# Performance work log

Measured on AMD Instinct MI355X. Metric: run time of the kernel, lower is better.

The kernel has to match this reference:

```python
import jax, jax.numpy as jnp
import numpy as np

NHEADS = 2
STRENGTH = 0.1
ZED = 8  # zone_embed_dim
STATE_DIM = 137
HID = 256
NBLOCKS = 4
BATCH = 131072


def _mha_seq1(q, k, v, in_w, in_b, out_w, out_b):
    """nn.MultiheadAttention (batch_first) with q,k,v of shape [B,1,E]."""
    B, _, E = q.shape
    hd = E // NHEADS
    Wq, Wk, Wv = in_w[:E], in_w[E:2 * E], in_w[2 * E:]
    bq, bk, bv = in_b[:E], in_b[E:2 * E], in_b[2 * E:]

    def heads(x, W, b):
        return (x @ W.T + b).reshape(B, -1, NHEADS, hd).transpose(0, 2, 1, 3)  # [B,H,1,hd]

    qh, kh, vh = heads(q, Wq, bq), heads(k, Wk, bk), heads(v, Wv, bv)
    scale = 1.0 / jnp.sqrt(jnp.asarray(hd, q.dtype))
    s = jnp.einsum('bhqd,bhkd->bhqk', qh, kh) * scale
    a = jax.nn.softmax(s, axis=-1)  # trivially ones for kv_len=1, kept for fidelity
    o = jnp.einsum('bhqk,bhkd->bhqd', a, vh).transpose(0, 2, 1, 3).reshape(B, -1, E)
    return o @ out_w.T + out_b


def setup_inputs() -> dict:
    key = jax.random.key(0)
    ks = jax.random.split(key, 20)
    S, H, N = STATE_DIM, HID, NBLOCKS
    ahd = S - ZED - 1  # 128

    def w(k, shape, fan_in):
        return jax.random.normal(k, shape, jnp.float32) * (1.0 / np.sqrt(fan_in))

    inp = {
        't': jax.random.uniform(ks[0], (1,), jnp.float32) * 24.0,
        'state': jax.random.normal(ks[1], (BATCH, S), jnp.float32),
        'W0': w(ks[2], (H, S + 2), S + 2), 'b0': jnp.zeros((H,), jnp.float32),
        'blkW1': w(ks[3], (N, H, H), H), 'blkb1': jnp.zeros((N, H), jnp.float32),
        'blkW2': w(ks[4], (N, H, H), H), 'blkb2': jnp.zeros((N, H), jnp.float32),
        'Wout': w(ks[5], (S, H), H), 'bout': jnp.zeros((S,), jnp.float32),
        'lm_in_w': w(ks[6], (3 * ZED, ZED), ZED), 'lm_in_b': jnp.zeros((3 * ZED,), jnp.float32),
        'lm_out_w': w(ks[7], (ZED, ZED), ZED), 'lm_out_b': jnp.zeros((ZED,), jnp.float32),
        'ta_in_w': w(ks[8], (3 * ahd, ahd), ahd), 'ta_in_b': jnp.zeros((3 * ahd,), jnp.float32),
        'ta_out_w': w(ks[9], (ahd, ahd), ahd), 'ta_out_b': jnp.zeros((ahd,), jnp.float32),
    }
    return inp


def reference(t, state, W0, b0, blkW1, blkb1, blkW2, blkb2, Wout, bout,
              lm_in_w, lm_in_b, lm_out_w, lm_out_b,
              ta_in_w, ta_in_b, ta_out_w, ta_out_b):
    B, S = state.shape
    ahd = S - ZED - 1
    two_pi_over_24 = 2.0 * jnp.pi / 24.0
    tv = jnp.concatenate([jnp.sin(t * two_pi_over_24), jnp.cos(t * two_pi_over_24)])  # [2]
    t_vec = jnp.broadcast_to(tv, (B, 2))

    # core dynamics MLP: Linear -> ReLU -> residual blocks -> Linear
    x = jnp.concatenate([state, t_vec], axis=-1)
    h = jax.nn.relu(x @ W0.T + b0)
    for i in range(blkW1.shape[0]):
        inner = jnp.tanh(h @ blkW1[i].T + blkb1[i]) @ blkW2[i].T + blkb2[i]
        h = jnp.tanh(h + inner)
    core = h @ Wout.T + bout

    # attention delta
    hs = state[:, :ahd]
    loc = state[:, ahd:ahd + ZED]
    mov = state[:, -1:]

    q_lm = jnp.broadcast_to(mov, (B, ZED))[:, None, :]
    loc_e = loc[:, None, :]
    enh_loc = _mha_seq1(q_lm, loc_e, loc_e, lm_in_w, lm_in_b, lm_out_w, lm_out_b)[:, 0]
    delta_loc = enh_loc - loc

    t_pad = jnp.concatenate([t_vec, jnp.zeros((B, ahd - 2), state.dtype)], axis=-1)[:, None, :]
    h_e = hs[:, None, :]
    enh_h = _mha_seq1(t_pad, h_e, h_e, ta_in_w, ta_in_b, ta_out_w, ta_out_b)[:, 0]
    delta_h = enh_h - hs

    delta = jnp.concatenate([delta_h, delta_loc, jnp.zeros_like(mov)], axis=-1)
    return core + STRENGTH * delta
```

## Files before the change

### kernel.cpp

```cpp
#include <hip/hip_runtime.h>

typedef __attribute__((ext_vector_type(8))) short short8;
typedef __attribute__((ext_vector_type(4))) float float4_;

#define SDIM    137
#define HID     256
#define K0PAD   160
#define KAUG    416
#define MTILE   64
#define NROWT   (MTILE / 16)
#define NTHR    512

#define SCLF 2.8853900817779268f
#define ISCL 0.34657359027997264f

struct __attribute__((aligned(8))) U2 { unsigned x, y; };

__device__ __forceinline__ unsigned short f2bf(float f) {
  union { float f; unsigned int i; } v; v.f = f;
  return (unsigned short)((v.i + 0x8000u) >> 16);
}
__device__ __forceinline__ unsigned pack_bf16(float a, float b) {
  union { float f; unsigned u; } ua, ub; ua.f = a; ub.f = b;
  return __builtin_amdgcn_perm(ub.u + 0x8000u, ua.u + 0x8000u, 0x07060302u);
}
__device__ __forceinline__ unsigned cvt_pk(float a, float b) {
  unsigned r;
  asm("v_cvt_pk_bf16_f32 %0, %1, %2" : "=v"(r) : "v"(a), "v"(b));
  return r;
}
__device__ __forceinline__ float lo_bf(unsigned p) {
  union { unsigned u; float f; } v; v.u = p << 16; return v.f;
}
__device__ __forceinline__ float hi_bf(unsigned p) {
  union { unsigned u; float f; } v; v.u = p & 0xFFFF0000u; return v.f;
}
__device__ __forceinline__ float stanh(float y) {
#if __has_builtin(__builtin_amdgcn_exp2f)
  float e = __builtin_amdgcn_exp2f(y);
#else
  float e = __expf(y * 0.6931471805599453f);
#endif
  float r = __builtin_amdgcn_rcpf(e + 1.f);
  return __builtin_fmaf(-2.f * SCLF, r, SCLF);
}
__device__ __forceinline__ int sidx(int row, int col) {
  return row * 256 + ((((col >> 3) ^ (row & 31)) << 3) | (col & 7));
}
__device__ __forceinline__ short8 ld_x(const unsigned short* __restrict__ X, int row, int c) {
  return *(const short8*)(X + row * 256 + (((c ^ (row & 31)) << 3)));
}

template<int NK, int LDB, int BOFF>
__device__ __forceinline__ void load_wa(const unsigned short* __restrict__ W,
                                        short8 (&wa)[NK][2], int colbase, int rm, int q)
{
  #pragma unroll
  for (int kb = 0; kb < NK; ++kb)
    #pragma unroll
    for (int mt = 0; mt < 2; ++mt)
      wa[kb][mt] = *(const short8*)(W + (size_t)(colbase + mt * 16 + rm) * LDB
                                      + BOFF + kb * 32 + q * 8);
}

template<int NK, class EPI>
__device__ __forceinline__ void gemm_f(const unsigned short* __restrict__ X,
                                       const short8 (&wa)[NK][2],
                                       int rm, int q, EPI epi)
{
  float4_ a[NROWT][2];
  #pragma unroll
  for (int nt = 0; nt < NROWT; ++nt) {
    short8 xb[NK];
    #pragma unroll
    for (int kb = 0; kb < NK; ++kb) xb[kb] = ld_x(X, nt * 16 + rm, kb * 4 + q);
    a[nt][0] = (float4_){0.f, 0.f, 0.f, 0.f};
    a[nt][1] = (float4_){0.f, 0.f, 0.f, 0.f};
    #pragma unroll
    for (int kb = 0; kb < NK; ++kb) {
      a[nt][0] = __builtin_amdgcn_mfma_f32_16x16x32_bf16(wa[kb][0], xb[kb], a[nt][0], 0, 0, 0);
      a[nt][1] = __builtin_amdgcn_mfma_f32_16x16x32_bf16(wa[kb][1], xb[kb], a[nt][1], 0, 0, 0);
    }
    if (nt > 0) epi(nt - 1, a[nt - 1]);
  }
  epi(NROWT - 1, a[NROWT - 1]);
}

template<int NK, int LDB, int BOFF>
__device__ __forceinline__ void mma_wact(const unsigned short* __restrict__ X,
                                         const unsigned short* __restrict__ W,
                                         float4_ (&acc)[2][NROWT], int lane, int colbase)
{
  const int q  = lane >> 4;
  const int rm = lane & 15;
  short8 wa[NK][2];
  load_wa<NK, LDB, BOFF>(W, wa, colbase, rm, q);
  #pragma unroll
  for (int kb = 0; kb < NK; ++kb) {
    short8 xb[NROWT];
    #pragma unroll
    for (int nt = 0; nt < NROWT; ++nt)
      xb[nt] = ld_x(X, nt * 16 + rm, kb * 4 + q);
    #pragma unroll
    for (int mt = 0; mt < 2; ++mt)
      #pragma unroll
      for (int nt = 0; nt < NROWT; ++nt)
        acc[mt][nt] = __builtin_amdgcn_mfma_f32_16x16x32_bf16(wa[kb][mt], xb[nt], acc[mt][nt], 0, 0, 0);
  }
}

#define PB_TA   256
#define PB_W0   385
#define PB_BLK  641
#define PB_END  1665

__global__ void prep_all(const float* __restrict__ t,
                         const float* __restrict__ W0,  const float* __restrict__ b0,
                         const float* __restrict__ Wout,const float* __restrict__ bout,
                         const float* __restrict__ lm_in_w, const float* __restrict__ lm_in_b,
                         const float* __restrict__ lm_out_w,const float* __restrict__ lm_out_b,
                         const float* __restrict__ ta_in_w, const float* __restrict__ ta_in_b,
                         const float* __restrict__ ta_out_w,const float* __restrict__ ta_out_b,
                         const float* __restrict__ blkW1, const float* __restrict__ blkW2,
                         unsigned short* __restrict__ W0p,  float* __restrict__ b0p,
                         unsigned short* __restrict__ Waug, float* __restrict__ baug,
                         unsigned short* __restrict__ W1b,  unsigned short* __restrict__ W2b)
{
  const int blk = blockIdx.x;
  const int tt  = threadIdx.x;

  if (blk < PB_TA) {
    int n = blk;
    if (tt < KAUG / 4) {
      int k0 = tt * 4;
      bool patch = (k0 >= 256) && ((n < 128 && k0 < 384) ||
                                   (n >= 128 && n < 136 && k0 >= 384 && k0 < 392));
      if (!patch) {
        U2 p;
        if (k0 < 256 && n < SDIM) {
          float4_ v = *(const float4_*)(Wout + (size_t)n * 256 + k0);
          p.x = pack_bf16(v[0] * ISCL, v[1] * ISCL);
          p.y = pack_bf16(v[2] * ISCL, v[3] * ISCL);
        } else { p.x = 0u; p.y = 0u; }
        *(U2*)(Waug + (size_t)n * KAUG + k0) = p;
      }
    }
  } else if (blk < PB_W0) {
    int b = blk - PB_TA;
    if (b < 128) {
      __shared__ float red[128];
      int n = b, s = tt;
      float dot = 0.f;
      #pragma unroll 8
      for (int r = 0; r < 128; ++r)
        dot += ta_out_w[n * 128 + r] * ta_in_w[(256 + r) * 128 + s];
      Waug[(size_t)n * KAUG + 256 + s] = f2bf(0.1f * (dot - (s == n ? 1.f : 0.f)));

      red[tt] = ta_out_w[n * 128 + tt] * ta_in_b[256 + tt];
      __syncthreads();
      if (tt < 64) {
        float p = red[tt] + red[tt + 64];
        for (int off = 32; off; off >>= 1) p += __shfl_down(p, off);
        if (tt == 0) baug[n] = bout[n] + 0.1f * (p + ta_out_b[n]);
      }
    } else {
      if (tt < 64) {
        int a = tt >> 3, c = tt & 7;
        float dot = 0.f;
        #pragma unroll
        for (int r = 0; r < 8; ++r)
          dot += lm_out_w[a * 8 + r] * lm_in_w[(16 + r) * 8 + c];
        Waug[(size_t)(128 + a) * KAUG + 384 + c] = f2bf(0.1f * (dot - (a == c ? 1.f : 0.f)));
      } else if (tt < 72) {
        int a = tt - 64;
        float dot = 0.f;
        #pragma unroll
        for (int r = 0; r < 8; ++r)
          dot += lm_out_w[a * 8 + r] * lm_in_b[16 + r];
        baug[128 + a] = bout[128 + a] + 0.1f * (dot + lm_out_b[a]);
      } else if (tt == 72) {
        baug[136] = bout[136];
        baug[137] = 0.f; baug[138] = 0.f; baug[139] = 0.f;
      }
    }
  } else if (blk < PB_BLK) {
    int n = blk - PB_W0;
    for (int k = tt; k < K0PAD; k += 128)
      W0p[n * K0PAD + k] = (k < SDIM) ? f2bf(W0[n * 139 + k] * SCLF) : (unsigned short)0;
    if (tt == 0) {
      float tv  = t[0];
      float ang = tv * (6.2831853071795864f / 24.0f);
      float sv = __sinf(ang), cv = __cosf(ang);
      b0p[n] = SCLF * (b0[n] + W0[n * 139 + 137] * sv + W0[n * 139 + 138] * cv);
    }
  } else {
    int i = ((blk - PB_BLK) * 128 + tt) * 4;
    const float* s; unsigned short* d;
    if (i < 262144) { s = blkW1 + i;          d = W1b + i; }
    else            { s = blkW2 + i - 262144; d = W2b + i - 262144; }
    float4_ v = *(const float4_*)s;
    U2 p; p.x = pack_bf16(v[0], v[1]); p.y = pack_bf16(v[2], v[3]);
    *(U2*)d = p;
  }
}


__global__ __launch_bounds__(NTHR, 4)
void fused_odefunc(
    const float* __restrict__ state,
    const unsigned short* __restrict__ W0p,
    const float* __restrict__ b0p,
    const unsigned short* __restrict__ blkW1,
    const float* __restrict__ blkb1,
    const unsigned short* __restrict__ blkW2,
    const float* __restrict__ blkb2,
    const unsigned short* __restrict__ Waug,
    const float* __restrict__ baug,
    float* __restrict__ out)
{
  __shared__ __align__(16) unsigned short ARENA[2 * MTILE * 256];
  unsigned short* H = ARENA;
  unsigned short* G = ARENA + MTILE * 256;
  float*          T = (float*)ARENA;

  const int tid  = threadIdx.x;
  const int lane = tid & 63;
  const int wave = tid >> 6;
  const int q    = lane >> 4;
  const int rm   = lane & 15;
  const int cb   = wave * 32;
  const int row0 = blockIdx.x * MTILE;

  #pragma unroll 2
  for (int qd = tid; qd < MTILE * (K0PAD / 4); qd += NTHR) {
    int m  = qd / (K0PAD / 4);
    int k0 = (qd - m * (K0PAD / 4)) * 4;
    const float* sp = state + (size_t)(row0 + m) * SDIM + k0;
    float f0 = (k0     < SDIM) ? sp[0] : 0.f;
    float f1 = (k0 + 1 < SDIM) ? sp[1] : 0.f;
    float f2 = (k0 + 2 < SDIM) ? sp[2] : 0.f;
    float f3 = (k0 + 3 < SDIM) ? sp[3] : 0.f;
    U2 p; p.x = cvt_pk(f0, f1); p.y = cvt_pk(f2, f3);
    *(U2*)(&G[sidx(m, k0)]) = p;
  }
  __syncthreads();

  {
    short8 wa[K0PAD / 32][2];
    load_wa<K0PAD / 32, K0PAD, 0>(W0p, wa, cb, rm, q);
    float4_ bias[2];
    #pragma unroll
    for (int mt = 0; mt < 2; ++mt) bias[mt] = *(const float4_*)(b0p + cb + mt * 16 + q * 4);
    gemm_f<K0PAD / 32>(G, wa, rm, q, [&](int nt, float4_ (&a2)[2]) {
      int row = nt * 16 + rm;
      #pragma unroll
      for (int mt = 0; mt < 2; ++mt) {
        int col0 = cb + mt * 16 + q * 4;
        float v0 = fmaxf(a2[mt][0] + bias[mt][0], 0.f);
        float v1 = fmaxf(a2[mt][1] + bias[mt][1], 0.f);
        float v2 = fmaxf(a2[mt][2] + bias[mt][2], 0.f);
        float v3 = fmaxf(a2[mt][3] + bias[mt][3], 0.f);
        U2 p; p.x = cvt_pk(v0, v1); p.y = cvt_pk(v2, v3);
        *(U2*)(&H[sidx(row, col0)]) = p;
      }
    });
  }
  __syncthreads();

  for (int blk = 0; blk < 4; ++blk) {
    const unsigned short* W1 = blkW1 + (size_t)blk * 65536;
    const float*          b1 = blkb1 + blk * 256;
    const unsigned short* W2 = blkW2 + (size_t)blk * 65536;
    const float*          b2 = blkb2 + blk * 256;

    {
      short8 wa[8][2];
      load_wa<8, 256, 0>(W1, wa, cb, rm, q);
      float4_ bb[2];
      #pragma unroll
      for (int mt = 0; mt < 2; ++mt) {
        float4_ t4 = *(const float4_*)(b1 + cb + mt * 16 + q * 4);
        bb[mt][0] = t4[0] * SCLF; bb[mt][1] = t4[1] * SCLF;
        bb[mt][2] = t4[2] * SCLF; bb[mt][3] = t4[3] * SCLF;
      }
      gemm_f<8>(H, wa, rm, q, [&](int nt, float4_ (&a2)[2]) {
        int row = nt * 16 + rm;
        #pragma unroll
        for (int mt = 0; mt < 2; ++mt) {
          int col0 = cb + mt * 16 + q * 4;
          float g0 = stanh(a2[mt][0] + bb[mt][0]);
          float g1 = stanh(a2[mt][1] + bb[mt][1]);
          float g2 = stanh(a2[mt][2] + bb[mt][2]);
          float g3 = stanh(a2[mt][3] + bb[mt][3]);
          U2 p; p.x = cvt_pk(g0, g1); p.y = cvt_pk(g2, g3);
          *(U2*)(&G[sidx(row, col0)]) = p;
        }
      });
    }
    __syncthreads();

    {
      short8 wa[8][2];
      load_wa<8, 256, 0>(W2, wa, cb, rm, q);
      float4_ bb[2];
      #pragma unroll
      for (int mt = 0; mt < 2; ++mt) {
        float4_ t4 = *(const float4_*)(b2 + cb + mt * 16 + q * 4);
        bb[mt][0] = t4[0] * SCLF; bb[mt][1] = t4[1] * SCLF;
        bb[mt][2] = t4[2] * SCLF; bb[mt][3] = t4[3] * SCLF;
      }
      gemm_f<8>(G, wa, rm, q, [&](int nt, float4_ (&a2)[2]) {
        int row = nt * 16 + rm;
        #pragma unroll
        for (int mt = 0; mt < 2; ++mt) {
          int col0 = cb + mt * 16 + q * 4;
          int idx = sidx(row, col0);
          U2 old = *(const U2*)(&H[idx]);
          float h0 = stanh(lo_bf(old.x) + a2[mt][0] + bb[mt][0]);
          float h1 = stanh(hi_bf(old.x) + a2[mt][1] + bb[mt][1]);
          float h2 = stanh(lo_bf(old.y) + a2[mt][2] + bb[mt][2]);
          float h3 = stanh(hi_bf(old.y) + a2[mt][3] + bb[mt][3]);
          U2 p; p.x = cvt_pk(h0, h1); p.y = cvt_pk(h2, h3);
          *(U2*)(&H[idx]) = p;
        }
      });
    }
    __syncthreads();
  }

  #pragma unroll 2
  for (int qd = tid; qd < MTILE * (K0PAD / 4); qd += NTHR) {
    int m  = qd / (K0PAD / 4);
    int k0 = (qd - m * (K0PAD / 4)) * 4;
    const float* sp = state + (size_t)(row0 + m) * SDIM + k0;
    float f0 = (k0     < SDIM) ? sp[0] : 0.f;
    float f1 = (k0 + 1 < SDIM) ? sp[1] : 0.f;
    float f2 = (k0 + 2 < SDIM) ? sp[2] : 0.f;
    float f3 = (k0 + 3 < SDIM) ? sp[3] : 0.f;
    U2 p; p.x = cvt_pk(f0, f1); p.y = cvt_pk(f2, f3);
    *(U2*)(&G[sidx(m, k0)]) = p;
  }

  float4_ acc[2][NROWT];
  #pragma unroll
  for (int mt = 0; mt < 2; ++mt)
    #pragma unroll
    for (int nt = 0; nt < NROWT; ++nt) acc[mt][nt] = (float4_){0.f, 0.f, 0.f, 0.f};
  if (cb < 160)
    mma_wact<8, KAUG, 0>(H, Waug, acc, lane, cb);
  __syncthreads();
  if (cb < 160)
    mma_wact<5, KAUG, 256>(G, Waug, acc, lane, cb);
  __syncthreads();
  if (cb < 160) {
    #pragma unroll
    for (int mt = 0; mt < 2; ++mt) {
      int col0 = cb + mt * 16 + q * 4;
      if (col0 <= 136) {
        float4_ bias = *(const float4_*)(baug + col0);
        #pragma unroll
        for (int nt = 0; nt < NROWT; ++nt) {
          int row = nt * 16 + rm;
          float4_ v;
          v[0] = acc[mt][nt][0] + bias[0];
          v[1] = acc[mt][nt][1] + bias[1];
          v[2] = acc[mt][nt][2] + bias[2];
          v[3] = acc[mt][nt][3] + bias[3];
          *(float4_*)(T + row * 140 + col0) = v;
        }
      }
    }
  }
  __syncthreads();

  float* obase = out + (size_t)row0 * SDIM;
  int r = tid / SDIM;
  int c = tid - r * SDIM;
  #pragma unroll 1
  for (int idx = tid; idx < MTILE * SDIM; idx += NTHR) {
    obase[idx] = T[r * 140 + c];
    c += NTHR - 3 * SDIM;
    r += 3;
    if (c >= SDIM) { c -= SDIM; r += 1; }
  }
}

extern "C" void kernel_launch(void* const* d_in, const int* in_sizes, int n_in,
                              void* d_out, int out_size, void* d_ws, size_t ws_size,
                              hipStream_t stream) {
  const float* t        = (const float*)d_in[0];
  const float* state    = (const float*)d_in[1];
  const float* W0       = (const float*)d_in[2];
  const float* b0       = (const float*)d_in[3];
  const float* blkW1    = (const float*)d_in[4];
  const float* blkb1    = (const float*)d_in[5];
  const float* blkW2    = (const float*)d_in[6];
  const float* blkb2    = (const float*)d_in[7];
  const float* Wout     = (const float*)d_in[8];
  const float* bout     = (const float*)d_in[9];
  const float* lm_in_w  = (const float*)d_in[10];
  const float* lm_in_b  = (const float*)d_in[11];
  const float* lm_out_w = (const float*)d_in[12];
  const float* lm_out_b = (const float*)d_in[13];
  const float* ta_in_w  = (const float*)d_in[14];
  const float* ta_in_b  = (const float*)d_in[15];
  const float* ta_out_w = (const float*)d_in[16];
  const float* ta_out_b = (const float*)d_in[17];

  char* ws = (char*)d_ws;
  unsigned short* W0p   = (unsigned short*)ws;
  float*          b0p   = (float*)(ws + 81920);
  unsigned short* Waug  = (unsigned short*)(ws + 82944);
  float*          baug  = (float*)(ws + 295936);
  unsigned short* W1b   = (unsigned short*)(ws + 296960);
  unsigned short* W2b   = (unsigned short*)(ws + 821248);

  prep_all<<<PB_END, 128, 0, stream>>>(t, W0, b0, Wout, bout,
                                       lm_in_w, lm_in_b, lm_out_w, lm_out_b,
                                       ta_in_w, ta_in_b, ta_out_w, ta_out_b,
                                       blkW1, blkW2,
                                       W0p, b0p, Waug, baug, W1b, W2b);

  int batch = in_sizes[1] / SDIM;
  fused_odefunc<<<batch / MTILE, NTHR, 0, stream>>>(
      state, W0p, b0p, W1b, blkb1, W2b, blkb2, Waug, baug,
      (float*)d_out);
}
```

Before: 478.6 us.

## Split GEMM K-loops into halves and write output directly from registers

Replaces the preloaded-full-K weight register arrays with a gemm_half helper that loads half of the weight fragments at a time, which lowers register pressure. Occupancy is now pinned with amdgpu_waves_per_eu(4,4). The final augmented GEMM also writes its results straight to global memory from the MFMA epilogue, dropping the LDS staging tile, an extra barrier and the separate coalesced copy loop. The cost is scattered, uncoalesced 4-byte global stores (rows of 137 floats) and weight fragments being reloaded per half.

```diff
diff --git a/kernel.cpp b/kernel.cpp
--- a/kernel.cpp
+++ b/kernel.cpp
@@ -51,62 +51,38 @@
   return *(const short8*)(X + row * 256 + (((c ^ (row & 31)) << 3)));
 }
 
-template<int NK, int LDB, int BOFF>
-__device__ __forceinline__ void load_wa(const unsigned short* __restrict__ W,
-                                        short8 (&wa)[NK][2], int colbase, int rm, int q)
+struct NoEpi { __device__ void operator()(int, float4_ (&)[2]) const {} };
+
+template<int KB0, int KN, int LDB, int BOFF, bool INIT, class EPI>
+__device__ __forceinline__ void gemm_half(const unsigned short* __restrict__ X,
+                                          const unsigned short* __restrict__ W,
+                                          float4_ (&a)[NROWT][2],
+                                          int rm, int q, int colbase, EPI epi)
 {
+  short8 wa[KN][2];
   #pragma unroll
-  for (int kb = 0; kb < NK; ++kb)
+  for (int kb = 0; kb < KN; ++kb)
     #pragma unroll
     for (int mt = 0; mt < 2; ++mt)
       wa[kb][mt] = *(const short8*)(W + (size_t)(colbase + mt * 16 + rm) * LDB
-                                      + BOFF + kb * 32 + q * 8);
-}
-
-template<int NK, class EPI>
-__device__ __forceinline__ void gemm_f(const unsigned short* __restrict__ X,
-                                       const short8 (&wa)[NK][2],
-                                       int rm, int q, EPI epi)
-{
-  float4_ a[NROWT][2];
+                                      + BOFF + (KB0 + kb) * 32 + q * 8);
   #pragma unroll
   for (int nt = 0; nt < NROWT; ++nt) {
-    short8 xb[NK];
+    short8 xb[KN];
     #pragma unroll
-    for (int kb = 0; kb < NK; ++kb) xb[kb] = ld_x(X, nt * 16 + rm, kb * 4 + q);
-    a[nt][0] = (float4_){0.f, 0.f, 0.f, 0.f};
-    a[nt][1] = (float4_){0.f, 0.f, 0.f, 0.f};
+    for (int kb = 0; kb < KN; ++kb) xb[kb] = ld_x(X, nt * 16 + rm, (KB0 + kb) * 4 + q);
+    if constexpr (INIT) {
+      a[nt][0] = (float4_){0.f, 0.f, 0.f, 0.f};
+      a[nt][1] = (float4_){0.f, 0.f, 0.f, 0.f};
+    }
     #pragma unroll
-    for (int kb = 0; kb < NK; ++kb) {
+    for (int kb = 0; kb < KN; ++kb) {
       a[nt][0] = __builtin_amdgcn_mfma_f32_16x16x32_bf16(wa[kb][0], xb[kb], a[nt][0], 0, 0, 0);
       a[nt][1] = __builtin_amdgcn_mfma_f32_16x16x32_bf16(wa[kb][1], xb[kb], a[nt][1], 0, 0, 0);
     }
     if (nt > 0) epi(nt - 1, a[nt - 1]);
   }
   epi(NROWT - 1, a[NROWT - 1]);
-}
-
-template<int NK, int LDB, int BOFF>
-__device__ __forceinline__ void mma_wact(const unsigned short* __restrict__ X,
-                                         const unsigned short* __restrict__ W,
-                                         float4_ (&acc)[2][NROWT], int lane, int colbase)
-{
-  const int q  = lane >> 4;
-  const int rm = lane & 15;
-  short8 wa[NK][2];
-  load_wa<NK, LDB, BOFF>(W, wa, colbase, rm, q);
-  #pragma unroll
-  for (int kb = 0; kb < NK; ++kb) {
-    short8 xb[NROWT];
-    #pragma unroll
-    for (int nt = 0; nt < NROWT; ++nt)
-      xb[nt] = ld_x(X, nt * 16 + rm, kb * 4 + q);
-    #pragma unroll
-    for (int mt = 0; mt < 2; ++mt)
-      #pragma unroll
-      for (int nt = 0; nt < NROWT; ++nt)
-        acc[mt][nt] = __builtin_amdgcn_mfma_f32_16x16x32_bf16(wa[kb][mt], xb[nt], acc[mt][nt], 0, 0, 0);
-  }
 }
 
 #define PB_TA   256
@@ -205,7 +181,8 @@
 }
 
 
-__global__ __launch_bounds__(NTHR, 4)
+__global__ __launch_bounds__(NTHR)
+__attribute__((amdgpu_waves_per_eu(4, 4)))
 void fused_odefunc(
     const float* __restrict__ state,
     const unsigned short* __restrict__ W0p,
@@ -221,7 +198,6 @@
   __shared__ __align__(16) unsigned short ARENA[2 * MTILE * 256];
   unsigned short* H = ARENA;
   unsigned short* G = ARENA + MTILE * 256;
-  float*          T = (float*)ARENA;
 
   const int tid  = threadIdx.x;
   const int lane = tid & 63;
@@ -245,13 +221,14 @@
   }
   __syncthreads();
 
+  float4_ a[NROWT][2];
+
   {
-    short8 wa[K0PAD / 32][2];
-    load_wa<K0PAD / 32, K0PAD, 0>(W0p, wa, cb, rm, q);
     float4_ bias[2];
     #pragma unroll
     for (int mt = 0; mt < 2; ++mt) bias[mt] = *(const float4_*)(b0p + cb + mt * 16 + q * 4);
-    gemm_f<K0PAD / 32>(G, wa, rm, q, [&](int nt, float4_ (&a2)[2]) {
+    gemm_half<0, 3, K0PAD, 0, true >(G, W0p, a, rm, q, cb, NoEpi{});
+    gemm_half<3, 2, K0PAD, 0, false>(G, W0p, a, rm, q, cb, [&](int nt, float4_ (&a2)[2]) {
       int row = nt * 16 + rm;
       #pragma unroll
       for (int mt = 0; mt < 2; ++mt) {
@@ -274,8 +251,6 @@
     const float*          b2 = blkb2 + blk * 256;
 
     {
-      short8 wa[8][2];
-      load_wa<8, 256, 0>(W1, wa, cb, rm, q);
       float4_ bb[2];
       #pragma unroll
       for (int mt = 0; mt < 2; ++mt) {
@@ -283,7 +258,8 @@
         bb[mt][0] = t4[0] * SCLF; bb[mt][1] = t4[1] * SCLF;
         bb[mt][2] = t4[2] * SCLF; bb[mt][3] = t4[3] * SCLF;
       }
-      gemm_f<8>(H, wa, rm, q, [&](int nt, float4_ (&a2)[2]) {
+      gemm_half<0, 4, 256, 0, true >(H, W1, a, rm, q, cb, NoEpi{});
+      gemm_half<4, 4, 256, 0, false>(H, W1, a, rm, q, cb, [&](int nt, float4_ (&a2)[2]) {
         int row = nt * 16 + rm;
         #pragma unroll
         for (int mt = 0; mt < 2; ++mt) {
@@ -300,8 +276,6 @@
     __syncthreads();
 
     {
-      short8 wa[8][2];
-      load_wa<8, 256, 0>(W2, wa, cb, rm, q);
       float4_ bb[2];
       #pragma unroll
       for (int mt = 0; mt < 2; ++mt) {
@@ -309,7 +283,8 @@
         bb[mt][0] = t4[0] * SCLF; bb[mt][1] = t4[1] * SCLF;
         bb[mt][2] = t4[2] * SCLF; bb[mt][3] = t4[3] * SCLF;
       }
-      gemm_f<8>(G, wa, rm, q, [&](int nt, float4_ (&a2)[2]) {
+      gemm_half<0, 4, 256, 0, true >(G, W2, a, rm, q, cb, NoEpi{});
+      gemm_half<4, 4, 256, 0, false>(G, W2, a, rm, q, cb, [&](int nt, float4_ (&a2)[2]) {
         int row = nt * 16 + rm;
         #pragma unroll
         for (int mt = 0; mt < 2; ++mt) {
@@ -341,47 +316,29 @@
     *(U2*)(&G[sidx(m, k0)]) = p;
   }
 
-  float4_ acc[2][NROWT];
-  #pragma unroll
-  for (int mt = 0; mt < 2; ++mt)
-    #pragma unroll
-    for (int nt = 0; nt < NROWT; ++nt) acc[mt][nt] = (float4_){0.f, 0.f, 0.f, 0.f};
-  if (cb < 160)
-    mma_wact<8, KAUG, 0>(H, Waug, acc, lane, cb);
-  __syncthreads();
-  if (cb < 160)
-    mma_wact<5, KAUG, 256>(G, Waug, acc, lane, cb);
+  if (cb < 160) {
+    gemm_half<0, 4, KAUG, 0, true >(H, Waug, a, rm, q, cb, NoEpi{});
+    gemm_half<4, 4, KAUG, 0, false>(H, Waug, a, rm, q, cb, NoEpi{});
+  }
   __syncthreads();
   if (cb < 160) {
-    #pragma unroll
-    for (int mt = 0; mt < 2; ++mt) {
-      int col0 = cb + mt * 16 + q * 4;
-      if (col0 <= 136) {
-        float4_ bias = *(const float4_*)(baug + col0);
-        #pragma unroll
-        for (int nt = 0; nt < NROWT; ++nt) {
-          int row = nt * 16 + rm;
-          float4_ v;
-          v[0] = acc[mt][nt][0] + bias[0];
-          v[1] = acc[mt][nt][1] + bias[1];
-          v[2] = acc[mt][nt][2] + bias[2];
-          v[3] = acc[mt][nt][3] + bias[3];
-          *(float4_*)(T + row * 140 + col0) = v;
+    gemm_half<0, 3, KAUG, 256, false>(G, Waug, a, rm, q, cb, NoEpi{});
+    gemm_half<3, 2, KAUG, 256, false>(G, Waug, a, rm, q, cb, [&](int nt, float4_ (&a2)[2]) {
+      float* orow = out + (size_t)(row0 + nt * 16 + rm) * SDIM;
+      #pragma unroll
+      for (int mt = 0; mt < 2; ++mt) {
+        int col0 = cb + mt * 16 + q * 4;
+        if (col0 < 136) {
+          float4_ b = *(const float4_*)(baug + col0);
+          orow[col0 + 0] = a2[mt][0] + b[0];
+          orow[col0 + 1] = a2[mt][1] + b[1];
+          orow[col0 + 2] = a2[mt][2] + b[2];
+          orow[col0 + 3] = a2[mt][3] + b[3];
+        } else if (col0 == 136) {
+          orow[136] = a2[mt][0] + baug[136];
         }
       }
-    }
-  }
-  __syncthreads();
-
-  float* obase = out + (size_t)row0 * SDIM;
-  int r = tid / SDIM;
-  int c = tid - r * SDIM;
-  #pragma unroll 1
-  for (int idx = tid; idx < MTILE * SDIM; idx += NTHR) {
-    obase[idx] = T[r * 140 + c];
-    c += NTHR - 3 * SDIM;
-    r += 3;
-    if (c >= SDIM) { c -= SDIM; r += 1; }
+    });
   }
 }
 
```

New measurement: 466.0 us. 1.03x faster.

## Double row tile and write outputs directly from accumulators

Applied to the files above, without the earlier changes.

Raises the per-block row tile from 64 to 128, so each block reuses every weight fetch across twice as many rows, and lowers occupancy to 2 waves per EU. The epilogue no longer stages results in shared memory with extra barriers. Each lane now writes its accumulator values plus bias straight to global memory as scalar stores. This removes two syncs and the LDS round trip, but the stores are strided and uncoalesced, shared memory doubles to 128KB per block, and register pressure per wave rises.

```diff
diff --git a/kernel.cpp b/kernel.cpp
--- a/kernel.cpp
+++ b/kernel.cpp
@@ -7,7 +7,7 @@
 #define HID     256
 #define K0PAD   160
 #define KAUG    416
-#define MTILE   64
+#define MTILE   128
 #define NROWT   (MTILE / 16)
 #define NTHR    512
 
@@ -205,7 +205,8 @@
 }
 
 
-__global__ __launch_bounds__(NTHR, 4)
+__global__ __launch_bounds__(NTHR, 2)
+__attribute__((amdgpu_waves_per_eu(2, 2)))
 void fused_odefunc(
     const float* __restrict__ state,
     const unsigned short* __restrict__ W0p,
@@ -221,7 +222,6 @@
   __shared__ __align__(16) unsigned short ARENA[2 * MTILE * 256];
   unsigned short* H = ARENA;
   unsigned short* G = ARENA + MTILE * 256;
-  float*          T = (float*)ARENA;
 
   const int tid  = threadIdx.x;
   const int lane = tid & 63;
@@ -349,39 +349,25 @@
   if (cb < 160)
     mma_wact<8, KAUG, 0>(H, Waug, acc, lane, cb);
   __syncthreads();
-  if (cb < 160)
+  if (cb < 160) {
     mma_wact<5, KAUG, 256>(G, Waug, acc, lane, cb);
-  __syncthreads();
-  if (cb < 160) {
-    #pragma unroll
-    for (int mt = 0; mt < 2; ++mt) {
-      int col0 = cb + mt * 16 + q * 4;
-      if (col0 <= 136) {
-        float4_ bias = *(const float4_*)(baug + col0);
-        #pragma unroll
-        for (int nt = 0; nt < NROWT; ++nt) {
-          int row = nt * 16 + rm;
-          float4_ v;
-          v[0] = acc[mt][nt][0] + bias[0];
-          v[1] = acc[mt][nt][1] + bias[1];
-          v[2] = acc[mt][nt][2] + bias[2];
-          v[3] = acc[mt][nt][3] + bias[3];
-          *(float4_*)(T + row * 140 + col0) = v;
+    #pragma unroll
+    for (int nt = 0; nt < NROWT; ++nt) {
+      float* orow = out + (size_t)(row0 + nt * 16 + rm) * SDIM;
+      #pragma unroll
+      for (int mt = 0; mt < 2; ++mt) {
+        int col0 = cb + mt * 16 + q * 4;
+        if (col0 < 136) {
+          float4_ b = *(const float4_*)(baug + col0);
+          orow[col0 + 0] = acc[mt][nt][0] + b[0];
+          orow[col0 + 1] = acc[mt][nt][1] + b[1];
+          orow[col0 + 2] = acc[mt][nt][2] + b[2];
+          orow[col0 + 3] = acc[mt][nt][3] + b[3];
+        } else if (col0 == 136) {
+          orow[136] = acc[mt][nt][0] + baug[136];
         }
       }
     }
-  }
-  __syncthreads();
-
-  float* obase = out + (size_t)row0 * SDIM;
-  int r = tid / SDIM;
-  int c = tid - r * SDIM;
-  #pragma unroll 1
-  for (int idx = tid; idx < MTILE * SDIM; idx += NTHR) {
-    obase[idx] = T[r * 140 + c];
-    c += NTHR - 3 * SDIM;
-    r += 3;
-    if (c >= SDIM) { c -= SDIM; r += 1; }
   }
 }
 
```

After: 454.0 us. 1.05x faster.
